# Optimization experiments

Measured on AMD Instinct MI355X. Metric: run time of the kernel, lower is better.

Reference implementation:

```python
import jax, jax.numpy as jnp
import numpy as np

DIM = 512
HEADS = 8
DIM_HEAD = 64
INNER = HEADS * DIM_HEAD
SCALE = DIM_HEAD ** -0.5


def setup_inputs() -> dict:
    key = jax.random.key(0)
    ks = jax.random.split(key, 6)
    b, n = 2, 2048
    x = jax.random.normal(ks[0], (b, n, DIM), dtype=jnp.float32)
    # torch Linear(dim, 3*inner, bias=False): store as [in, out] for x @ W
    w_qkv = jax.random.normal(ks[1], (DIM, 3 * INNER), dtype=jnp.float32) * (DIM ** -0.5)
    # Conv2d(heads, heads, 1, bias=False) weights squeezed to [out_h, in_h]
    w_pre = jax.random.normal(ks[2], (HEADS, HEADS), dtype=jnp.float32) * (HEADS ** -0.5)
    w_post = jax.random.normal(ks[3], (HEADS, HEADS), dtype=jnp.float32) * (HEADS ** -0.5)
    w_out = jax.random.normal(ks[4], (INNER, DIM), dtype=jnp.float32) * (INNER ** -0.5)
    b_out = jax.random.normal(ks[5], (DIM,), dtype=jnp.float32) * 0.01
    return {"x": x, "w_qkv": w_qkv, "w_pre": w_pre, "w_post": w_post,
            "w_out": w_out, "b_out": b_out}


def reference(x, w_qkv, w_pre, w_post, w_out, b_out):
    b, n, _ = x.shape
    qkv = x @ w_qkv  # [b, n, 3*inner]
    q, k, v = jnp.split(qkv, 3, axis=-1)
    # b n (h d) -> b h n d
    split_heads = lambda t: t.reshape(b, n, HEADS, DIM_HEAD).transpose(0, 2, 1, 3)
    q, k, v = split_heads(q), split_heads(k), split_heads(v)
    dots = jnp.einsum('bhid,bhjd->bhij', q, k) * SCALE
    # pre-softmax talking-heads: 1x1 conv over the head axis
    dots = jnp.einsum('gh,bhij->bgij', w_pre, dots)
    attn = jax.nn.softmax(dots, axis=-1)
    # post-softmax talking-heads mix
    attn = jnp.einsum('gh,bhij->bgij', w_post, attn)
    out = jnp.einsum('bhij,bhjd->bhid', attn, v)
    out = out.transpose(0, 2, 1, 3).reshape(b, n, INNER)  # b h n d -> b n (h d)
    return out @ w_out + b_out
```

## Files before the change

kernel.cpp:

```cpp
#include <hip/hip_runtime.h>
#include <hip/hip_bf16.h>

typedef unsigned short ushort_t;
typedef __attribute__((ext_vector_type(8))) short short8;
typedef __attribute__((ext_vector_type(4))) short short4v;
typedef __attribute__((ext_vector_type(4))) float floatx4;
typedef __attribute__((ext_vector_type(2))) float floatx2;

#define MFMA16(a, b, c) __builtin_amdgcn_mfma_f32_16x16x32_bf16(a, b, c, 0, 0, 0)

__device__ __forceinline__ float bf2f(ushort_t u) {
    unsigned int v = ((unsigned int)u) << 16;
    return __int_as_float((int)v);
}
__device__ __forceinline__ ushort_t f2bf(float f) {
    unsigned int x = (unsigned int)__float_as_int(f);
    unsigned int r = (x + 0x7FFFu + ((x >> 16) & 1u)) >> 16;
    return (ushort_t)r;
}

__global__ __launch_bounds__(256) void k_cvt(const floatx4* __restrict__ src,
                                             short4v* __restrict__ dst, int n4) {
    int i = blockIdx.x * 256 + threadIdx.x;
    if (i < n4) {
        floatx4 v = src[i];
        short4v o;
        o[0] = (short)f2bf(v[0]);
        o[1] = (short)f2bf(v[1]);
        o[2] = (short)f2bf(v[2]);
        o[3] = (short)f2bf(v[3]);
        dst[i] = o;
    }
}

__global__ __launch_bounds__(256) void k_transpose_cvt(const float* __restrict__ src,
                                                       ushort_t* __restrict__ dst, int R, int C) {
    __shared__ float t[32][33];
    int tx = threadIdx.x & 31, ty = threadIdx.x >> 5;
    int r0 = blockIdx.y * 32, c0 = blockIdx.x * 32;
    for (int y = ty; y < 32; y += 8) t[y][tx] = src[(r0 + y) * C + c0 + tx];
    __syncthreads();
    for (int y = ty; y < 32; y += 8) dst[(c0 + y) * R + r0 + tx] = f2bf(t[tx][y]);
}

__global__ __launch_bounds__(256, 3) void k_qkv(const ushort_t* __restrict__ x,
                                                const ushort_t* __restrict__ wt,
                                                ushort_t* __restrict__ qs,
                                                ushort_t* __restrict__ ks,
                                                ushort_t* __restrict__ vt) {
    __shared__ __align__(16) ushort_t st[9216];
    const int tid = threadIdx.x, lane = tid & 63, wv = tid >> 6;
    const int col = lane & 15, quad = lane >> 4;
    const int which = blockIdx.x >> 3, hh = blockIdx.x & 7;
    const int c0 = blockIdx.x * 64;
    const int absrow0 = blockIdx.y * 128;
    const int bb = blockIdx.y >> 4, n0 = (blockIdx.y & 15) * 128;
    const int hidx = bb * 8 + hh;
    const int row0 = absrow0 + wv * 32;
    floatx4 acc[2][4];
#pragma unroll
    for (int i = 0; i < 2; i++)
#pragma unroll
        for (int j = 0; j < 4; j++) acc[i][j] = (floatx4){0.f, 0.f, 0.f, 0.f};
    for (int k0 = 0; k0 < 512; k0 += 32) {
        const int ko = k0 + quad * 8;
        short8 a0 = *(const short8*)&x[(row0 + col) * 512 + ko];
        short8 a1 = *(const short8*)&x[(row0 + 16 + col) * 512 + ko];
        short8 b0 = *(const short8*)&wt[(c0 + col) * 512 + ko];
        short8 b1 = *(const short8*)&wt[(c0 + 16 + col) * 512 + ko];
        short8 b2 = *(const short8*)&wt[(c0 + 32 + col) * 512 + ko];
        short8 b3 = *(const short8*)&wt[(c0 + 48 + col) * 512 + ko];
        acc[0][0] = MFMA16(a0, b0, acc[0][0]);
        acc[0][1] = MFMA16(a0, b1, acc[0][1]);
        acc[0][2] = MFMA16(a0, b2, acc[0][2]);
        acc[0][3] = MFMA16(a0, b3, acc[0][3]);
        acc[1][0] = MFMA16(a1, b0, acc[1][0]);
        acc[1][1] = MFMA16(a1, b1, acc[1][1]);
        acc[1][2] = MFMA16(a1, b2, acc[1][2]);
        acc[1][3] = MFMA16(a1, b3, acc[1][3]);
    }
    const float qscale = (which == 0) ? 0.125f : 1.0f;
#pragma unroll
    for (int i = 0; i < 2; i++)
#pragma unroll
        for (int j = 0; j < 4; j++)
#pragma unroll
            for (int r = 0; r < 4; r++) {
                int il = wv * 32 + i * 16 + quad * 4 + r;
                int cl = j * 16 + col;
                ushort_t hv = f2bf(acc[i][j][r] * qscale);
                if (which == 2) st[cl * 136 + il] = hv;
                else            st[il * 72 + cl] = hv;
            }
    __syncthreads();
    if (which < 2) {
        ushort_t* dst = (which == 0) ? qs : ks;
#pragma unroll
        for (int s = tid; s < 1024; s += 256) {
            int rr = s >> 3, dc = (s & 7) * 8;
            *(short8*)&dst[(hidx * 2048 + n0 + rr) * 64 + dc] = *(const short8*)&st[rr * 72 + dc];
        }
    } else {
#pragma unroll
        for (int s = tid; s < 1024; s += 256) {
            int d = s >> 4, nc = (s & 15) * 8;
            *(short8*)&vt[(hidx * 64 + d) * 2048 + n0 + nc] = *(const short8*)&st[d * 136 + nc];
        }
    }
}

__global__ __launch_bounds__(512, 1) void k_attn(const ushort_t* __restrict__ qs,
                                                 const ushort_t* __restrict__ ks,
                                                 const ushort_t* __restrict__ vt,
                                                 const float* __restrict__ w_pre,
                                                 const float* __restrict__ w_post,
                                                 const ushort_t* __restrict__ wot,
                                                 const float* __restrict__ bias,
                                                 float* __restrict__ out) {
    __shared__ __align__(16) ushort_t qlds[8 * 16 * 72];
    __shared__ __align__(16) ushort_t U[8 * 16 * 140];
    __shared__ float lred[8][8][16];
    __shared__ float linv[8][16];
    const int tid = threadIdx.x, lane = tid & 63, wv = tid >> 6;
    const int col = lane & 15, quad = lane >> 4;
    const int b = blockIdx.y, n0 = blockIdx.x * 16;
    const int e = wv;

    for (int c = tid; c < 1024; c += 512) {
        int hh = c >> 7, rem = c & 127, ii = rem >> 3, dc = (rem & 7) * 8;
        *(short8*)&qlds[(hh * 16 + ii) * 72 + dc] =
            *(const short8*)&qs[((b * 8 + hh) * 2048 + n0 + ii) * 64 + dc];
    }
    __syncthreads();

    floatx4 Oa[8][4];
    float Lacc[8][4];
#pragma unroll
    for (int g = 0; g < 8; g++) {
#pragma unroll
        for (int nt = 0; nt < 4; nt++) Oa[g][nt] = (floatx4){0.f, 0.f, 0.f, 0.f};
#pragma unroll
        for (int r = 0; r < 4; r++) Lacc[g][r] = 0.f;
    }

    for (int tile = 0; tile < 16; tile++) {
        const int j0 = tile * 128;
        const int jw = j0 + wv * 16;
        floatx4 S[8];
#pragma unroll
        for (int h = 0; h < 8; h++) {
            const ushort_t* qb = &qlds[(h * 16 + col) * 72 + quad * 8];
            short8 a0 = *(const short8*)&qb[0];
            short8 a1 = *(const short8*)&qb[32];
            const ushort_t* kb = &ks[((b * 8 + h) * 2048 + jw + col) * 64 + quad * 8];
            short8 b0 = *(const short8*)&kb[0];
            short8 b1 = *(const short8*)&kb[32];
            floatx4 a = (floatx4){0.f, 0.f, 0.f, 0.f};
            a = MFMA16(a0, b0, a);
            a = MFMA16(a1, b1, a);
            S[h] = a;
        }
#pragma unroll
        for (int g = 0; g < 8; g++)
#pragma unroll
            for (int r2 = 0; r2 < 2; r2++) {
                floatx2 s = (floatx2){0.f, 0.f};
#pragma unroll
                for (int h = 0; h < 8; h++) {
                    floatx2 sv = (floatx2){S[h][2 * r2], S[h][2 * r2 + 1]};
                    s += sv * w_pre[g * 8 + h];
                }
                float u0 = __expf(s.x), u1 = __expf(s.y);
                Lacc[g][2 * r2] += u0;
                Lacc[g][2 * r2 + 1] += u1;
                U[(g * 16 + quad * 4 + 2 * r2) * 140 + wv * 16 + col] = f2bf(u0);
                U[(g * 16 + quad * 4 + 2 * r2 + 1) * 140 + wv * 16 + col] = f2bf(u1);
            }
        __syncthreads();
#pragma unroll
        for (int k2 = 0; k2 < 4; k2++) {
            short8 bf[4];
#pragma unroll
            for (int nt = 0; nt < 4; nt++)
                bf[nt] = *(const short8*)&vt[((b * 8 + e) * 64 + nt * 16 + col) * 2048 + j0 +
                                             k2 * 32 + quad * 8];
#pragma unroll
            for (int g = 0; g < 8; g++) {
                short8 af = *(const short8*)&U[(g * 16 + col) * 140 + k2 * 32 + quad * 8];
#pragma unroll
                for (int nt = 0; nt < 4; nt++) Oa[g][nt] = MFMA16(af, bf[nt], Oa[g][nt]);
            }
        }
        __syncthreads();
    }

#pragma unroll
    for (int g = 0; g < 8; g++)
#pragma unroll
        for (int r = 0; r < 4; r++) {
            float v = Lacc[g][r];
            v += __shfl_xor(v, 1, 64);
            v += __shfl_xor(v, 2, 64);
            v += __shfl_xor(v, 4, 64);
            v += __shfl_xor(v, 8, 64);
            if (col == 0) lred[wv][g][quad * 4 + r] = v;
        }
    __syncthreads();
    if (tid < 128) {
        int g = tid >> 4, ii = tid & 15;
        float l = 0.f;
#pragma unroll
        for (int w2 = 0; w2 < 8; w2++) l += lred[w2][g][ii];
        linv[g][ii] = 1.0f / l;
    }
    __syncthreads();
    float coef[8][4];
#pragma unroll
    for (int g = 0; g < 8; g++) {
        float wqe = w_post[e * 8 + g];
#pragma unroll
        for (int r = 0; r < 4; r++) coef[g][r] = wqe * linv[g][quad * 4 + r];
    }
    ushort_t* oline = U;
#pragma unroll
    for (int nt = 0; nt < 4; nt++)
#pragma unroll
        for (int r = 0; r < 4; r++) {
            float o = 0.f;
#pragma unroll
            for (int g = 0; g < 8; g++) o = fmaf(coef[g][r], Oa[g][nt][r], o);
            oline[(quad * 4 + r) * 520 + e * 64 + nt * 16 + col] = f2bf(o);
        }
    __syncthreads();
#pragma unroll
    for (int nt = 0; nt < 4; nt++) {
        floatx4 acc = (floatx4){0.f, 0.f, 0.f, 0.f};
        const int c = wv * 64 + nt * 16 + col;
#pragma unroll
        for (int k2 = 0; k2 < 16; k2++) {
            short8 af = *(const short8*)&oline[col * 520 + k2 * 32 + quad * 8];
            short8 bf = *(const short8*)&wot[c * 512 + k2 * 32 + quad * 8];
            acc = MFMA16(af, bf, acc);
        }
        float bz = bias[c];
#pragma unroll
        for (int r = 0; r < 4; r++)
            out[(b * 2048 + n0 + quad * 4 + r) * 512 + c] = acc[r] + bz;
    }
}

extern "C" void kernel_launch(void* const* d_in, const int* in_sizes, int n_in,
                              void* d_out, int out_size, void* d_ws, size_t ws_size,
                              hipStream_t stream) {
    const float* x = (const float*)d_in[0];
    const float* w_qkv = (const float*)d_in[1];
    const float* w_pre = (const float*)d_in[2];
    const float* w_post = (const float*)d_in[3];
    const float* w_out = (const float*)d_in[4];
    const float* b_out = (const float*)d_in[5];
    char* ws = (char*)d_ws;
    ushort_t* qs = (ushort_t*)(ws);
    ushort_t* ks = (ushort_t*)(ws + (4u << 20));
    ushort_t* vt = (ushort_t*)(ws + (8u << 20));
    ushort_t* xb = (ushort_t*)(ws + (12u << 20));
    ushort_t* wt = (ushort_t*)(ws + (16u << 20));
    ushort_t* wot = (ushort_t*)(ws + (16u << 20) + 1572864u);
    float* out = (float*)d_out;

    k_cvt<<<dim3(2048), dim3(256), 0, stream>>>((const floatx4*)x, (short4v*)xb, 524288);
    k_transpose_cvt<<<dim3(48, 16), dim3(256), 0, stream>>>(w_qkv, wt, 512, 1536);
    k_transpose_cvt<<<dim3(16, 16), dim3(256), 0, stream>>>(w_out, wot, 512, 512);
    k_qkv<<<dim3(24, 32), dim3(256), 0, stream>>>(xb, wt, qs, ks, vt);
    k_attn<<<dim3(128, 2), dim3(512), 0, stream>>>(qs, ks, vt, w_pre, w_post, wot, b_out, out);
}
```

Before: 321.3 us.

## Restructure attention as two-pass with register-resident talking-heads mixing and split-K waves

Rewrites the attention kernel into a two-pass scheme. The first pass computes the softmax denominators. The second recomputes the scores, normalises them and applies the post-softmax head mix in registers, then feeds the result directly into K=16 MFMAs against V. Waves now split the key dimension instead of heads and reduce their partial outputs through LDS. This removes the LDS round trip of the exp tile and the per-tile barriers, at the cost of computing QK^T twice and using more registers for Q fragments, weights and 32 output accumulators per wave. Workgroups shrink to 256 threads.

```diff
diff --git a/kernel.cpp b/kernel.cpp
--- a/kernel.cpp
+++ b/kernel.cpp
@@ -5,9 +5,21 @@
 typedef __attribute__((ext_vector_type(8))) short short8;
 typedef __attribute__((ext_vector_type(4))) short short4v;
 typedef __attribute__((ext_vector_type(4))) float floatx4;
-typedef __attribute__((ext_vector_type(2))) float floatx2;
 
 #define MFMA16(a, b, c) __builtin_amdgcn_mfma_f32_16x16x32_bf16(a, b, c, 0, 0, 0)
+
+#if __has_builtin(__builtin_amdgcn_mfma_f32_16x16x16bf16_1k)
+#define MFMA16K16(a, b, c) __builtin_amdgcn_mfma_f32_16x16x16bf16_1k(a, b, c, 0, 0, 0)
+#else
+static __device__ __forceinline__ floatx4 mfma_bf16_k16(short4v a, short4v b, floatx4 c) {
+    floatx4 d;
+    asm volatile("s_nop 2\n\tv_mfma_f32_16x16x16_bf16 %0, %1, %2, %3"
+                 : "=v"(d)
+                 : "v"(a), "v"(b), "v"(c));
+    return d;
+}
+#define MFMA16K16(a, b, c) mfma_bf16_k16(a, b, c)
+#endif
 
 __device__ __forceinline__ float bf2f(ushort_t u) {
     unsigned int v = ((unsigned int)u) << 16;
@@ -109,7 +121,7 @@
     }
 }
 
-__global__ __launch_bounds__(512, 1) void k_attn(const ushort_t* __restrict__ qs,
+__global__ __launch_bounds__(256, 1) void k_attn(const ushort_t* __restrict__ qs,
                                                  const ushort_t* __restrict__ ks,
                                                  const ushort_t* __restrict__ vt,
                                                  const float* __restrict__ w_pre,
@@ -117,125 +129,145 @@
                                                  const ushort_t* __restrict__ wot,
                                                  const float* __restrict__ bias,
                                                  float* __restrict__ out) {
-    __shared__ __align__(16) ushort_t qlds[8 * 16 * 72];
-    __shared__ __align__(16) ushort_t U[8 * 16 * 140];
-    __shared__ float lred[8][8][16];
-    __shared__ float linv[8][16];
+    __shared__ float wlds[128];
+    __shared__ float lred[4][8][16];
+    __shared__ float linv_l[8][16];
+    __shared__ float slotf[4 * 16 * 68];
+    __shared__ __align__(16) ushort_t oline[16 * 520];
     const int tid = threadIdx.x, lane = tid & 63, wv = tid >> 6;
     const int col = lane & 15, quad = lane >> 4;
     const int b = blockIdx.y, n0 = blockIdx.x * 16;
-    const int e = wv;
-
-    for (int c = tid; c < 1024; c += 512) {
-        int hh = c >> 7, rem = c & 127, ii = rem >> 3, dc = (rem & 7) * 8;
-        *(short8*)&qlds[(hh * 16 + ii) * 72 + dc] =
-            *(const short8*)&qs[((b * 8 + hh) * 2048 + n0 + ii) * 64 + dc];
-    }
-    __syncthreads();
-
-    floatx4 Oa[8][4];
-    float Lacc[8][4];
+
+    if (tid < 128) wlds[tid] = (tid < 64) ? w_pre[tid] : w_post[tid - 64];
+    __syncthreads();
+    float wp[64], wq[64];
+#pragma unroll
+    for (int i = 0; i < 64; i++) { wp[i] = wlds[i]; wq[i] = wlds[64 + i]; }
+
+    short8 Qf[8][2];
+#pragma unroll
+    for (int h = 0; h < 8; h++) {
+        const ushort_t* qb = &qs[((b * 8 + h) * 2048 + n0 + col) * 64 + quad * 8];
+        Qf[h][0] = *(const short8*)&qb[0];
+        Qf[h][1] = *(const short8*)&qb[32];
+    }
+
+    float Lacc[8];
+#pragma unroll
+    for (int g = 0; g < 8; g++) Lacc[g] = 0.f;
+    for (int st = 0; st < 32; st++) {
+        const int jw = wv * 512 + st * 16;
+        floatx4 P2[8];
+#pragma unroll
+        for (int g = 0; g < 8; g++) P2[g] = (floatx4){0.f, 0.f, 0.f, 0.f};
+#pragma unroll
+        for (int h = 0; h < 8; h++) {
+            const ushort_t* kb = &ks[((b * 8 + h) * 2048 + jw + col) * 64 + quad * 8];
+            short8 k0 = *(const short8*)&kb[0];
+            short8 k1 = *(const short8*)&kb[32];
+            floatx4 sh = (floatx4){0.f, 0.f, 0.f, 0.f};
+            sh = MFMA16(k0, Qf[h][0], sh);
+            sh = MFMA16(k1, Qf[h][1], sh);
+#pragma unroll
+            for (int g = 0; g < 8; g++) P2[g] += sh * wp[g * 8 + h];
+        }
+#pragma unroll
+        for (int g = 0; g < 8; g++) {
+            floatx4 p = P2[g];
+            Lacc[g] += __expf(p[0]) + __expf(p[1]) + __expf(p[2]) + __expf(p[3]);
+        }
+    }
 #pragma unroll
     for (int g = 0; g < 8; g++) {
-#pragma unroll
-        for (int nt = 0; nt < 4; nt++) Oa[g][nt] = (floatx4){0.f, 0.f, 0.f, 0.f};
-#pragma unroll
-        for (int r = 0; r < 4; r++) Lacc[g][r] = 0.f;
-    }
-
-    for (int tile = 0; tile < 16; tile++) {
-        const int j0 = tile * 128;
-        const int jw = j0 + wv * 16;
-        floatx4 S[8];
-#pragma unroll
-        for (int h = 0; h < 8; h++) {
-            const ushort_t* qb = &qlds[(h * 16 + col) * 72 + quad * 8];
-            short8 a0 = *(const short8*)&qb[0];
-            short8 a1 = *(const short8*)&qb[32];
-            const ushort_t* kb = &ks[((b * 8 + h) * 2048 + jw + col) * 64 + quad * 8];
-            short8 b0 = *(const short8*)&kb[0];
-            short8 b1 = *(const short8*)&kb[32];
-            floatx4 a = (floatx4){0.f, 0.f, 0.f, 0.f};
-            a = MFMA16(a0, b0, a);
-            a = MFMA16(a1, b1, a);
-            S[h] = a;
-        }
-#pragma unroll
-        for (int g = 0; g < 8; g++)
-#pragma unroll
-            for (int r2 = 0; r2 < 2; r2++) {
-                floatx2 s = (floatx2){0.f, 0.f};
-#pragma unroll
-                for (int h = 0; h < 8; h++) {
-                    floatx2 sv = (floatx2){S[h][2 * r2], S[h][2 * r2 + 1]};
-                    s += sv * w_pre[g * 8 + h];
-                }
-                float u0 = __expf(s.x), u1 = __expf(s.y);
-                Lacc[g][2 * r2] += u0;
-                Lacc[g][2 * r2 + 1] += u1;
-                U[(g * 16 + quad * 4 + 2 * r2) * 140 + wv * 16 + col] = f2bf(u0);
-                U[(g * 16 + quad * 4 + 2 * r2 + 1) * 140 + wv * 16 + col] = f2bf(u1);
-            }
-        __syncthreads();
-#pragma unroll
-        for (int k2 = 0; k2 < 4; k2++) {
-            short8 bf[4];
-#pragma unroll
-            for (int nt = 0; nt < 4; nt++)
-                bf[nt] = *(const short8*)&vt[((b * 8 + e) * 64 + nt * 16 + col) * 2048 + j0 +
-                                             k2 * 32 + quad * 8];
-#pragma unroll
-            for (int g = 0; g < 8; g++) {
-                short8 af = *(const short8*)&U[(g * 16 + col) * 140 + k2 * 32 + quad * 8];
-#pragma unroll
-                for (int nt = 0; nt < 4; nt++) Oa[g][nt] = MFMA16(af, bf[nt], Oa[g][nt]);
-            }
-        }
-        __syncthreads();
-    }
-
-#pragma unroll
-    for (int g = 0; g < 8; g++)
-#pragma unroll
-        for (int r = 0; r < 4; r++) {
-            float v = Lacc[g][r];
-            v += __shfl_xor(v, 1, 64);
-            v += __shfl_xor(v, 2, 64);
-            v += __shfl_xor(v, 4, 64);
-            v += __shfl_xor(v, 8, 64);
-            if (col == 0) lred[wv][g][quad * 4 + r] = v;
-        }
+        float v = Lacc[g];
+        v += __shfl_xor(v, 16, 64);
+        v += __shfl_xor(v, 32, 64);
+        if (lane < 16) lred[wv][g][lane] = v;
+    }
     __syncthreads();
     if (tid < 128) {
         int g = tid >> 4, ii = tid & 15;
-        float l = 0.f;
-#pragma unroll
-        for (int w2 = 0; w2 < 8; w2++) l += lred[w2][g][ii];
-        linv[g][ii] = 1.0f / l;
-    }
-    __syncthreads();
-    float coef[8][4];
-#pragma unroll
-    for (int g = 0; g < 8; g++) {
-        float wqe = w_post[e * 8 + g];
-#pragma unroll
-        for (int r = 0; r < 4; r++) coef[g][r] = wqe * linv[g][quad * 4 + r];
-    }
-    ushort_t* oline = U;
-#pragma unroll
-    for (int nt = 0; nt < 4; nt++)
-#pragma unroll
-        for (int r = 0; r < 4; r++) {
-            float o = 0.f;
-#pragma unroll
-            for (int g = 0; g < 8; g++) o = fmaf(coef[g][r], Oa[g][nt][r], o);
-            oline[(quad * 4 + r) * 520 + e * 64 + nt * 16 + col] = f2bf(o);
-        }
-    __syncthreads();
-#pragma unroll
-    for (int nt = 0; nt < 4; nt++) {
+        float l = lred[0][g][ii] + lred[1][g][ii] + lred[2][g][ii] + lred[3][g][ii];
+        linv_l[g][ii] = 1.0f / l;
+    }
+    __syncthreads();
+    float linvr[8];
+#pragma unroll
+    for (int g = 0; g < 8; g++) linvr[g] = linv_l[g][col];
+
+    floatx4 O[8][4];
+#pragma unroll
+    for (int e = 0; e < 8; e++)
+#pragma unroll
+        for (int nt = 0; nt < 4; nt++) O[e][nt] = (floatx4){0.f, 0.f, 0.f, 0.f};
+
+    for (int st = 0; st < 32; st++) {
+        const int jw = wv * 512 + st * 16;
+        floatx4 P2[8];
+#pragma unroll
+        for (int g = 0; g < 8; g++) P2[g] = (floatx4){0.f, 0.f, 0.f, 0.f};
+#pragma unroll
+        for (int h = 0; h < 8; h++) {
+            const ushort_t* kb = &ks[((b * 8 + h) * 2048 + jw + col) * 64 + quad * 8];
+            short8 k0 = *(const short8*)&kb[0];
+            short8 k1 = *(const short8*)&kb[32];
+            floatx4 sh = (floatx4){0.f, 0.f, 0.f, 0.f};
+            sh = MFMA16(k0, Qf[h][0], sh);
+            sh = MFMA16(k1, Qf[h][1], sh);
+#pragma unroll
+            for (int g = 0; g < 8; g++) P2[g] += sh * wp[g * 8 + h];
+        }
+        float Un[8][4];
+#pragma unroll
+        for (int g = 0; g < 8; g++)
+#pragma unroll
+            for (int r = 0; r < 4; r++) Un[g][r] = __expf(P2[g][r]) * linvr[g];
+        short4v Af[8];
+#pragma unroll
+        for (int e = 0; e < 8; e++) {
+#pragma unroll
+            for (int r = 0; r < 4; r++) {
+                float a = 0.f;
+#pragma unroll
+                for (int g = 0; g < 8; g++) a = fmaf(wq[e * 8 + g], Un[g][r], a);
+                Af[e][r] = (short)f2bf(a);
+            }
+        }
+#pragma unroll
+        for (int e = 0; e < 8; e++) {
+            const ushort_t* vb = &vt[((b * 8 + e) * 64 + col) * 2048 + jw + quad * 4];
+#pragma unroll
+            for (int nt = 0; nt < 4; nt++) {
+                short4v bf = *(const short4v*)&vb[nt * 16 * 2048];
+                O[e][nt] = MFMA16K16(Af[e], bf, O[e][nt]);
+            }
+        }
+    }
+
+#pragma unroll 1
+    for (int e = 0; e < 8; e++) {
+#pragma unroll
+        for (int nt = 0; nt < 4; nt++)
+#pragma unroll
+            for (int r = 0; r < 4; r++)
+                slotf[wv * 1088 + (quad * 4 + r) * 68 + nt * 16 + col] = O[e][nt][r];
+        __syncthreads();
+        {
+            int i = tid >> 4, d0 = (tid & 15) * 4;
+#pragma unroll
+            for (int k = 0; k < 4; k++) {
+                int d = d0 + k;
+                float s = slotf[0 * 1088 + i * 68 + d] + slotf[1 * 1088 + i * 68 + d] +
+                          slotf[2 * 1088 + i * 68 + d] + slotf[3 * 1088 + i * 68 + d];
+                oline[i * 520 + e * 64 + d] = f2bf(s);
+            }
+        }
+        __syncthreads();
+    }
+#pragma unroll
+    for (int ct = 0; ct < 8; ct++) {
         floatx4 acc = (floatx4){0.f, 0.f, 0.f, 0.f};
-        const int c = wv * 64 + nt * 16 + col;
+        const int c = wv * 128 + ct * 16 + col;
 #pragma unroll
         for (int k2 = 0; k2 < 16; k2++) {
             short8 af = *(const short8*)&oline[col * 520 + k2 * 32 + quad * 8];
@@ -271,5 +303,5 @@
     k_transpose_cvt<<<dim3(48, 16), dim3(256), 0, stream>>>(w_qkv, wt, 512, 1536);
     k_transpose_cvt<<<dim3(16, 16), dim3(256), 0, stream>>>(w_out, wot, 512, 512);
     k_qkv<<<dim3(24, 32), dim3(256), 0, stream>>>(xb, wt, qs, ks, vt);
-    k_attn<<<dim3(128, 2), dim3(512), 0, stream>>>(qs, ks, vt, w_pre, w_post, wot, b_out, out);
-}
+    k_attn<<<dim3(128, 2), dim3(256), 0, stream>>>(qs, ks, vt, w_pre, w_post, wot, b_out, out);
+}
```

Measured after the change: 1.007 ms. +213.5%, slower.
